# Kernel tuning notes

Measured on AMD Instinct MI355X. Metric: run time of the kernel, lower is better.

## Reference

```python
import jax, jax.numpy as jnp
import numpy as np

EPS = 1e-5  # BatchNorm2d eps
NEG_SLOPE = 0.01  # LeakyReLU default


def _cconv_bn_act(x, W, b, g, beta):
    # Complex 1x1 conv + per-part BatchNorm (batch stats) + LeakyReLU.
    # x: [B,2,C,F,T]; W: [2,C,C] (real, imag); b, g, beta: [2,C]
    xr, xi = x[:, 0], x[:, 1]
    yr = (jnp.einsum('oc,bcft->boft', W[0], xr)
          - jnp.einsum('oc,bcft->boft', W[1], xi) + b[0][None, :, None, None])
    yi = (jnp.einsum('oc,bcft->boft', W[0], xi)
          + jnp.einsum('oc,bcft->boft', W[1], xr) + b[1][None, :, None, None])

    def bn(y, gg, bb):
        mu = y.mean(axis=(0, 2, 3), keepdims=True)
        var = y.var(axis=(0, 2, 3), keepdims=True)  # biased, as torch BN normalization
        return (y - mu) / jnp.sqrt(var + EPS) * gg[None, :, None, None] + bb[None, :, None, None]

    yr = jax.nn.leaky_relu(bn(yr, g[0], beta[0]), NEG_SLOPE)
    yi = jax.nn.leaky_relu(bn(yi, g[1], beta[1]), NEG_SLOPE)
    return jnp.stack((yr, yi), axis=1)


def _complex_attn(q, k, v):
    # q,k,v: [B,2,N,D]; magnitude-based scores, softmax over dim=1 of [B,N,N]
    # (faithful to nn.Softmax(dim=1) applied to a 3-D score tensor).
    qr, qi = q[:, 0], q[:, 1]
    kr, ki = k[:, 0], k[:, 1]
    sr = jnp.einsum('bnd,bmd->bnm', qr, kr) + jnp.einsum('bnd,bmd->bnm', qi, ki)
    si = jnp.einsum('bnd,bmd->bnm', qi, kr) - jnp.einsum('bnd,bmd->bnm', qr, ki)
    a = jax.nn.softmax(jnp.sqrt(sr * sr + si * si), axis=1)
    outr = jnp.einsum('bnm,bmd->bnd', a, v[:, 0])
    outi = jnp.einsum('bnm,bmd->bnd', a, v[:, 1])
    return jnp.stack((outr, outi), axis=1)


def _forward(P, Q, W, b, g, beta):
    B, _, C, F, T = P.shape
    # --- Time-axis attention: tokens = T frames, feature dim = C*F ---
    qt = _cconv_bn_act(Q, W[0], b[0], g[0], beta[0])
    kt = _cconv_bn_act(P, W[1], b[1], g[1], beta[1])
    vt = _cconv_bn_act(P, W[2], b[2], g[2], beta[2])

    def to_time(x):  # [B,2,C,F,T] -> [B,2,T,C*F]
        return x.reshape(B, 2, C * F, T).transpose(0, 1, 3, 2)

    ot = _complex_attn(to_time(qt), to_time(kt), to_time(vt))
    ot = ot.transpose(0, 1, 3, 2).reshape(B, 2, C, F, T)

    # --- Freq-axis attention: tokens = F bins, feature dim = C*T ---
    qf = _cconv_bn_act(Q, W[3], b[3], g[3], beta[3])
    kf = _cconv_bn_act(P, W[4], b[4], g[4], beta[4])
    vf = _cconv_bn_act(P, W[5], b[5], g[5], beta[5])

    def to_freq(x):  # [B,2,C,F,T] -> [B,2,F,C*T]
        return x.transpose(0, 1, 3, 2, 4).reshape(B, 2, F, C * T)

    of = _complex_attn(to_freq(qf), to_freq(kf), to_freq(vf))
    of = of.reshape(B, 2, F, C, T).transpose(0, 1, 3, 2, 4)

    # Combine the two attention axes (truncated top-level module; see notes).
    return ot + of


def setup_inputs():
    key = jax.random.key(0)
    ks = jax.random.split(key, 4)
    B, C, F, T = 2, 64, 256, 256
    P = jax.random.normal(ks[0], (B, 2, C, F, T), dtype=jnp.float32)
    Q = jax.random.normal(ks[1], (B, 2, C, F, T), dtype=jnp.float32)
    # 6 branches: [time-q, time-k, time-v, freq-q, freq-k, freq-v]
    W = jax.random.normal(ks[2], (6, 2, C, C), dtype=jnp.float32) / np.sqrt(C).astype(np.float32)
    b = jax.random.normal(ks[3], (6, 2, C), dtype=jnp.float32) * 0.01
    g = jnp.ones((6, 2, C), dtype=jnp.float32)
    beta = jnp.zeros((6, 2, C), dtype=jnp.float32)
    return {"P": P, "Q": Q, "W": W, "b": b, "g": g, "beta": beta}


def reference(P, Q, W, b, g, beta):
    return _forward(P, Q, W, b, g, beta)
```

## Files before the change

kernel.cpp:

```cpp
#include <hip/hip_runtime.h>
#include <math.h>

#define SS 65536
#define PLANE 4194304
#define TEN_ELEMS 16777216
#define NBUCKET 64

typedef __bf16 bf16x8 __attribute__((ext_vector_type(8)));
typedef __bf16 bf16x4v __attribute__((ext_vector_type(4)));
typedef float  f32x4  __attribute__((ext_vector_type(4)));

__device__ inline f32x4 mfma16(bf16x8 a, bf16x8 b, f32x4 c) {
  return __builtin_amdgcn_mfma_f32_16x16x32_bf16(a, b, c, 0, 0, 0);
}
__device__ inline bf16x8 neg8(bf16x8 v) {
  union { bf16x8 b; unsigned u[4]; } t; t.b = v;
#pragma unroll
  for (int i = 0; i < 4; ++i) t.u[i] ^= 0x80008000u;
  return t.b;
}
__device__ inline float bnlrelu(float v, float sc, float sh) {
  float t = fmaf(v, sc, sh);
  return t > 0.f ? t : 0.01f * t;
}

__device__ inline int swz(int r, int g) {
  return r * 40 + (((g ^ (r >> 2) ^ (r >> 4)) & 3) << 3);
}

__global__ __launch_bounds__(256) void cconv_mfma(
    const float* __restrict__ x, const float* __restrict__ Wj,
    const float* __restrict__ bias, float* __restrict__ y,
    float* __restrict__ part)
{
  __shared__ __align__(16) __bf16 sBh[64 * 136];
  __shared__ __align__(16) __bf16 sBl[64 * 136];
  const int tid = threadIdx.x;
  const int b = blockIdx.y;
  const int s0 = blockIdx.x << 6;
  const int bkt = (blockIdx.x & (NBUCKET - 1)) * 768;
  const int w = tid >> 6, q = (tid >> 4) & 3, ln = tid & 15;

  bf16x8 ah[2][4], al[2][4];
#pragma unroll
  for (int mt = 0; mt < 2; ++mt) {
    int row = w * 32 + mt * 16 + ln;
    int po = row >> 6, co = row & 63;
#pragma unroll
    for (int ks = 0; ks < 4; ++ks) {
      bf16x8 vh, vl;
#pragma unroll
      for (int j = 0; j < 8; ++j) {
        int k = ks * 32 + q * 8 + j;
        int pi = k >> 6, c = k & 63;
        float v = Wj[((po ^ pi) << 12) + co * 64 + c];
        if (po == 0 && pi == 1) v = -v;
        __bf16 h = (__bf16)v;
        vh[j] = h;
        vl[j] = (__bf16)(v - (float)h);
      }
      ah[mt][ks] = vh; al[mt][ks] = vl;
    }
  }

#pragma unroll
  for (int ph = 0; ph < 2; ++ph) {
    int pc = ph * 64 + (tid & 63);
    const float* rowp = x + (size_t)(b * 128 + pc) * SS + s0;
#pragma unroll
    for (int sh2 = 0; sh2 < 2; ++sh2)
#pragma unroll
      for (int sc2 = 0; sc2 < 2; ++sc2) {
        int sl = ((tid >> 6) << 3) + sh2 * 32 + sc2 * 4;
        float4 rd = *(const float4*)&rowp[sl];
        float vv[4] = {rd.x, rd.y, rd.z, rd.w};
#pragma unroll
        for (int e = 0; e < 4; ++e) {
          __bf16 h = (__bf16)vv[e];
          sBh[(sl + e) * 136 + pc] = h;
          sBl[(sl + e) * 136 + pc] = (__bf16)(vv[e] - (float)h);
        }
      }
  }
  __syncthreads();

  f32x4 zero = {0.f, 0.f, 0.f, 0.f};
  f32x4 acc[2][4];
#pragma unroll
  for (int mt = 0; mt < 2; ++mt)
#pragma unroll
    for (int nt = 0; nt < 4; ++nt) acc[mt][nt] = zero;

#pragma unroll
  for (int ks = 0; ks < 4; ++ks) {
    bf16x8 bh[4], bl[4];
#pragma unroll
    for (int nt = 0; nt < 4; ++nt) {
      int off = (nt * 16 + ln) * 136 + ks * 32 + q * 8;
      bh[nt] = *(const bf16x8*)&sBh[off];
      bl[nt] = *(const bf16x8*)&sBl[off];
    }
#pragma unroll
    for (int mt = 0; mt < 2; ++mt)
#pragma unroll
      for (int nt = 0; nt < 4; ++nt) {
        acc[mt][nt] = mfma16(ah[mt][ks], bh[nt], acc[mt][nt]);
        acc[mt][nt] = mfma16(ah[mt][ks], bl[nt], acc[mt][nt]);
        acc[mt][nt] = mfma16(al[mt][ks], bh[nt], acc[mt][nt]);
      }
  }

#pragma unroll
  for (int mt = 0; mt < 2; ++mt) {
    int rowb = w * 32 + mt * 16 + q * 4;
#pragma unroll
    for (int r = 0; r < 4; ++r) {
      float bv = bias[rowb + r];
      float vs[4];
      float sm = 0.f, sq = 0.f;
#pragma unroll
      for (int nt = 0; nt < 4; ++nt) {
        float v = acc[mt][nt][r] + bv;
        vs[nt] = v; sm += v; sq += v * v;
      }
#pragma unroll
      for (int off = 1; off < 16; off <<= 1) {
        sm += __shfl_xor(sm, off, 64);
        sq += __shfl_xor(sq, off, 64);
      }
      if (ln == 0) {
        atomicAdd(&part[bkt + (rowb + r) * 2 + 0], sm);
        atomicAdd(&part[bkt + (rowb + r) * 2 + 1], sq);
      }
#pragma unroll
      for (int nt = 0; nt < 4; ++nt)
        y[(size_t)((b << 7) + rowb + r) * SS + s0 + nt * 16 + ln] = vs[nt];
    }
  }
}

__global__ void bn_finalize(const float* __restrict__ buckets,
                            const float* __restrict__ g,
                            const float* __restrict__ beta, int goff,
                            float* __restrict__ scale, float* __restrict__ shift)
{
  int i = blockIdx.x * 256 + threadIdx.x;
  if (i >= 384) return;
  int role = i >> 7, pc = i & 127;
  float sm = 0.f, sq = 0.f;
  const float* bp = buckets + role * 256 + pc * 2;
#pragma unroll 4
  for (int k = 0; k < NBUCKET; ++k) {
    sm += bp[k * 768 + 0];
    sq += bp[k * 768 + 1];
  }
  const float inv = 1.f / 131072.f;
  float mu = sm * inv;
  float var = sq * inv - mu * mu;
  float istd = rsqrtf(var + 1e-5f);
  float gg = g[goff + role * 128 + pc];
  float bb = beta[goff + role * 128 + pc];
  float sc = gg * istd;
  scale[i] = sc;
  shift[i] = bb - mu * sc;
}

__global__ __launch_bounds__(256) void qk_prep(
    float* __restrict__ y0, float* __restrict__ y1,
    const float* __restrict__ scale, const float* __restrict__ shift, int freq)
{
  const int g = blockIdx.x;
  const int b2p = blockIdx.y;
  const int role = blockIdx.z;
  float* y = role ? y1 : y0;
  const int p = b2p & 1;
  const int c = g >> 3;
  const float sc = scale[role * 128 + p * 64 + c];
  const float sh = shift[role * 128 + p * 64 + c];
  const int tid = threadIdx.x;
  const size_t base = (size_t)b2p * PLANE + (size_t)g * 8192;
  __bf16* yo = (__bf16*)y;

  float v[32];
  if (freq) {
    size_t off = base + (size_t)tid * 32;
#pragma unroll
    for (int r = 0; r < 8; ++r) {
      float4 t4 = *(const float4*)&y[off + r * 4];
      v[r * 4 + 0] = t4.x; v[r * 4 + 1] = t4.y;
      v[r * 4 + 2] = t4.z; v[r * 4 + 3] = t4.w;
    }
    size_t ob = off * 2;
#pragma unroll
    for (int r = 0; r < 4; ++r) {
      bf16x8 hv, lv;
#pragma unroll
      for (int e = 0; e < 8; ++e) {
        float t = bnlrelu(v[r * 8 + e], sc, sh);
        __bf16 hh = (__bf16)t;
        hv[e] = hh; lv[e] = (__bf16)(t - (float)hh);
      }
      *(bf16x8*)&yo[ob + r * 8]      = hv;
      *(bf16x8*)&yo[ob + 32 + r * 8] = lv;
    }
  } else {
    __shared__ __align__(16) float sT[32 * 256];
#pragma unroll
    for (int r = 0; r < 8; ++r) {
      int u = tid + (r << 8);
      int tok4 = u & 63, j = u >> 6;
      float4 t4 = *(const float4*)&y[base + j * 256 + tok4 * 4];
      *(float4*)&sT[j * 256 + ((tok4 ^ j) << 2)] = t4;
    }
    __syncthreads();
    const int tok = tid;
#pragma unroll
    for (int j = 0; j < 32; ++j)
      v[j] = sT[j * 256 + (((tok >> 2) ^ j) << 2) + (tok & 3)];
    size_t ob = (base + (size_t)tok * 32) * 2;
#pragma unroll
    for (int r = 0; r < 4; ++r) {
      bf16x8 hv, lv;
#pragma unroll
      for (int e = 0; e < 8; ++e) {
        float t = bnlrelu(v[r * 8 + e], sc, sh);
        __bf16 hh = (__bf16)t;
        hv[e] = hh; lv[e] = (__bf16)(t - (float)hh);
      }
      *(bf16x8*)&yo[ob + r * 8]      = hv;
      *(bf16x8*)&yo[ob + 32 + r * 8] = lv;
    }
  }
}

__global__ __launch_bounds__(256) void score_mfma(
    const __bf16* __restrict__ qt, const __bf16* __restrict__ kt,
    float* __restrict__ SR, float* __restrict__ SI, int freq)
{
  __shared__ __align__(16) __bf16 sQh[2 * 128 * 40], sQl[2 * 128 * 40];
  __shared__ __align__(16) __bf16 sKh[2 * 64 * 40],  sKl[2 * 64 * 40];
  const int tid = threadIdx.x;
  const int sid = blockIdx.x + (blockIdx.y << 3) + (blockIdx.z << 8);
  const int kk = sid & 7, tt = sid >> 3;
  const int n0 = (kk & 1) << 7;
  const int b  = (kk >> 1) & 1;
  const int m0 = (tt & 3) << 6;
  const int d0 = (((kk >> 2) << 4) + (tt >> 2)) << 9;
  const int g0 = d0 >> 5;
  const int w = tid >> 6, q4 = (tid >> 4) & 3, ln = tid & 15;
  const size_t pb = (size_t)(b * 2) * (2 * PLANE);

  f32x4 zero = {0.f, 0.f, 0.f, 0.f};
  f32x4 accr[2][4], acci[2][4];
#pragma unroll
  for (int st = 0; st < 2; ++st)
#pragma unroll
    for (int mt = 0; mt < 4; ++mt) { accr[st][mt] = zero; acci[st][mt] = zero; }

  for (int ch = 0; ch < 16; ++ch) {
    const int g = g0 + ch;
    int Gq, Gk, Gstep;
    if (freq) {
      int cc = g >> 3, gg = g & 7;
      Gq = cc * 2048 + n0 * 8 + gg;
      Gk = cc * 2048 + m0 * 8 + gg;
      Gstep = 8;
    } else {
      Gq = g * 256 + n0;
      Gk = g * 256 + m0;
      Gstep = 1;
    }
#pragma unroll
    for (int r = 0; r < 4; ++r) {
      int u = tid + (r << 8);
      int g_ = u & 3, tok = (u >> 2) & 127, p = u >> 9;
      size_t a = pb + (size_t)p * (2 * PLANE) +
                 (size_t)(Gq + tok * Gstep) * 64 + (g_ << 3);
      int dst = swz(p * 128 + tok, g_);
      *(bf16x8*)&sQh[dst] = *(const bf16x8*)&qt[a];
      *(bf16x8*)&sQl[dst] = *(const bf16x8*)&qt[a + 32];
    }
#pragma unroll
    for (int r = 0; r < 2; ++r) {
      int u = tid + (r << 8);
      int g_ = u & 3, tok = (u >> 2) & 63, p = u >> 8;
      size_t a = pb + (size_t)p * (2 * PLANE) +
                 (size_t)(Gk + tok * Gstep) * 64 + (g_ << 3);
      int dst = swz(p * 64 + tok, g_);
      *(bf16x8*)&sKh[dst] = *(const bf16x8*)&kt[a];
      *(bf16x8*)&sKl[dst] = *(const bf16x8*)&kt[a + 32];
    }
    __syncthreads();

    bf16x8 qh[2][2], ql2[2][2], nqh[2], nql[2];
#pragma unroll
    for (int st = 0; st < 2; ++st) {
      int tokn = w * 32 + st * 16 + ln;
#pragma unroll
      for (int p = 0; p < 2; ++p) {
        int off = swz(p * 128 + tokn, q4);
        qh[st][p]  = *(const bf16x8*)&sQh[off];
        ql2[st][p] = *(const bf16x8*)&sQl[off];
      }
      nqh[st] = neg8(qh[st][0]);
      nql[st] = neg8(ql2[st][0]);
    }
#pragma unroll
    for (int mt = 0; mt < 4; ++mt) {
      int tk = mt * 16 + ln;
      int offr = swz(tk, q4), offi = swz(64 + tk, q4);
      bf16x8 krh = *(const bf16x8*)&sKh[offr];
      bf16x8 krl = *(const bf16x8*)&sKl[offr];
      bf16x8 kih = *(const bf16x8*)&sKh[offi];
      bf16x8 kil = *(const bf16x8*)&sKl[offi];
#pragma unroll
      for (int st = 0; st < 2; ++st) {
        f32x4 ar = accr[st][mt], ai = acci[st][mt];
        ar = mfma16(qh[st][0], krh, ar);
        ar = mfma16(qh[st][0], krl, ar);
        ar = mfma16(ql2[st][0], krh, ar);
        ar = mfma16(qh[st][1], kih, ar);
        ar = mfma16(qh[st][1], kil, ar);
        ar = mfma16(ql2[st][1], kih, ar);
        ai = mfma16(qh[st][1], krh, ai);
        ai = mfma16(qh[st][1], krl, ai);
        ai = mfma16(ql2[st][1], krh, ai);
        ai = mfma16(nqh[st], kih, ai);
        ai = mfma16(nqh[st], kil, ai);
        ai = mfma16(nql[st], kih, ai);
        accr[st][mt] = ar; acci[st][mt] = ai;
      }
    }
    __syncthreads();
  }

#pragma unroll
  for (int st = 0; st < 2; ++st)
#pragma unroll
    for (int mt = 0; mt < 4; ++mt)
#pragma unroll
      for (int r = 0; r < 4; ++r) {
        int n = n0 + w * 32 + st * 16 + q4 * 4 + r;
        int m = m0 + mt * 16 + ln;
        int idx = (b << 16) + (n << 8) + m;
        atomicAdd(&SR[idx], accr[st][mt][r]);
        atomicAdd(&SI[idx], acci[st][mt][r]);
      }
}

__global__ __launch_bounds__(256) void softmax_kernel(
    const float* __restrict__ sr, const float* __restrict__ si,
    float* __restrict__ am)
{
  const int m = blockIdx.x & 255;
  const int b = blockIdx.x >> 8;
  const int n = threadIdx.x;
  const int idx = (b << 16) + (n << 8) + m;
  float vr = sr[idx], vi = si[idx];
  float mag = sqrtf(vr * vr + vi * vi);
  __shared__ float wmax[4];
  __shared__ float wsum[4];
  float mx = mag;
  #pragma unroll
  for (int off = 1; off < 64; off <<= 1)
    mx = fmaxf(mx, __shfl_xor(mx, off, 64));
  if ((threadIdx.x & 63) == 0) wmax[threadIdx.x >> 6] = mx;
  __syncthreads();
  mx = fmaxf(fmaxf(wmax[0], wmax[1]), fmaxf(wmax[2], wmax[3]));
  float e = expf(mag - mx);
  float sm = e;
  #pragma unroll
  for (int off = 1; off < 64; off <<= 1)
    sm += __shfl_xor(sm, off, 64);
  if ((threadIdx.x & 63) == 0) wsum[threadIdx.x >> 6] = sm;
  __syncthreads();
  float tot = wsum[0] + wsum[1] + wsum[2] + wsum[3];
  am[idx] = e / tot;
}

__global__ __launch_bounds__(256) void vt_convert(
    const float* __restrict__ y2, const float* __restrict__ scale,
    const float* __restrict__ shift, __bf16* __restrict__ vh,
    __bf16* __restrict__ vl)
{
  size_t i = ((size_t)blockIdx.x * 256 + threadIdx.x) << 2;
  int idx = 256 + (int)((i >> 16) & 127);
  float sc = scale[idx], sh = shift[idx];
  float4 v = *(const float4*)&y2[i];
  float vv[4] = {v.x, v.y, v.z, v.w};
  bf16x4v h, l;
#pragma unroll
  for (int e = 0; e < 4; ++e) {
    float t = bnlrelu(vv[e], sc, sh);
    __bf16 hh = (__bf16)t;
    h[e] = hh; l[e] = (__bf16)(t - (float)hh);
  }
  *(bf16x4v*)&vh[i] = h;
  *(bf16x4v*)&vl[i] = l;
}

__global__ __launch_bounds__(256) void vt_transpose(
    const float* __restrict__ y2, const float* __restrict__ scale,
    const float* __restrict__ shift, __bf16* __restrict__ vh,
    __bf16* __restrict__ vl)
{
  __shared__ float sT[64 * 65];
  const int tid = threadIdx.x;
  const int bpc = blockIdx.y;
  const int bp = bpc >> 6, c = bpc & 63;
  const int f0 = (blockIdx.x >> 2) << 6, t0 = (blockIdx.x & 3) << 6;
  const float sc = scale[256 + (bp & 1) * 64 + c];
  const float sh = shift[256 + (bp & 1) * 64 + c];
  const float* src = y2 + (size_t)bp * PLANE + (size_t)c * SS;
#pragma unroll
  for (int r = 0; r < 4; ++r) {
    int fl = (tid >> 4) + (r << 4);
    int tl = (tid & 15) << 2;
    float4 v = *(const float4*)&src[(f0 + fl) * 256 + t0 + tl];
    sT[fl * 65 + tl + 0] = bnlrelu(v.x, sc, sh);
    sT[fl * 65 + tl + 1] = bnlrelu(v.y, sc, sh);
    sT[fl * 65 + tl + 2] = bnlrelu(v.z, sc, sh);
    sT[fl * 65 + tl + 3] = bnlrelu(v.w, sc, sh);
  }
  __syncthreads();
  __bf16* dsth = vh + (((size_t)bp * 16384 + c * 256) << 8);
  __bf16* dstl = vl + (((size_t)bp * 16384 + c * 256) << 8);
#pragma unroll
  for (int r = 0; r < 4; ++r) {
    int tl = (tid >> 4) + (r << 4);
    int fl = (tid & 15) << 2;
    bf16x4v h, l;
#pragma unroll
    for (int e = 0; e < 4; ++e) {
      float vv = sT[(fl + e) * 65 + tl];
      __bf16 hh = (__bf16)vv;
      h[e] = hh; l[e] = (__bf16)(vv - (float)hh);
    }
    *(bf16x4v*)&dsth[(size_t)(t0 + tl) * 256 + f0 + fl] = h;
    *(bf16x4v*)&dstl[(size_t)(t0 + tl) * 256 + f0 + fl] = l;
  }
}

__global__ __launch_bounds__(256) void av_mfma(
    const float* __restrict__ am, const __bf16* __restrict__ vth,
    const __bf16* __restrict__ vtl, float* __restrict__ out, int freq)
{
  __shared__ __align__(16) char smem[55296];
  __bf16* sVh = (__bf16*)smem;
  __bf16* sVl = (__bf16*)(smem + 18432);
  __bf16* sAh = (__bf16*)(smem + 36864);
  __bf16* sAl = (__bf16*)(smem + 46080);
  const int tid = threadIdx.x;
  const int d0 = blockIdx.x << 7;
  const int n0 = blockIdx.y << 6;
  const int bp = blockIdx.z, b = bp >> 1;
  const int w = tid >> 6, q = (tid >> 4) & 3, ln = tid & 15;
  const __bf16* vhp = vth + (((size_t)bp * 16384 + d0) << 8);
  const __bf16* vlp = vtl + (((size_t)bp * 16384 + d0) << 8);
  float* op = out + (size_t)bp * PLANE;

  f32x4 zero = {0.f, 0.f, 0.f, 0.f};
  f32x4 acc[2][4];
#pragma unroll
  for (int mt = 0; mt < 2; ++mt)
#pragma unroll
    for (int nt = 0; nt < 4; ++nt) acc[mt][nt] = zero;

  for (int m0 = 0; m0 < 256; m0 += 64) {
#pragma unroll
    for (int r = 0; r < 4; ++r) {
      int u = tid + (r << 8);
      int dl = u >> 3, g = (u & 7) << 3;
      *(bf16x8*)&sVh[dl * 72 + g] = *(const bf16x8*)&vhp[dl * 256 + m0 + g];
      *(bf16x8*)&sVl[dl * 72 + g] = *(const bf16x8*)&vlp[dl * 256 + m0 + g];
    }
#pragma unroll
    for (int r = 0; r < 4; ++r) {
      int u = tid + (r << 8);
      int mj = (u & 15) << 2, nl = u >> 4;
      float4 v4 = *(const float4*)&am[(b << 16) + ((n0 + nl) << 8) + m0 + mj];
      float vv[4] = {v4.x, v4.y, v4.z, v4.w};
      bf16x4v h, l;
#pragma unroll
      for (int e = 0; e < 4; ++e) {
        __bf16 hh = (__bf16)vv[e];
        h[e] = hh; l[e] = (__bf16)(vv[e] - (float)hh);
      }
      *(bf16x4v*)&sAh[nl * 72 + mj] = h;
      *(bf16x4v*)&sAl[nl * 72 + mj] = l;
    }
    __syncthreads();

#pragma unroll
    for (int ks = 0; ks < 2; ++ks) {
      bf16x8 vhf[2], vlf[2], ahf[4], alf[4];
#pragma unroll
      for (int mt = 0; mt < 2; ++mt) {
        int off = (w * 32 + mt * 16 + ln) * 72 + ks * 32 + q * 8;
        vhf[mt] = *(const bf16x8*)&sVh[off];
        vlf[mt] = *(const bf16x8*)&sVl[off];
      }
#pragma unroll
      for (int nt = 0; nt < 4; ++nt) {
        int off = (nt * 16 + ln) * 72 + ks * 32 + q * 8;
        ahf[nt] = *(const bf16x8*)&sAh[off];
        alf[nt] = *(const bf16x8*)&sAl[off];
      }
#pragma unroll
      for (int mt = 0; mt < 2; ++mt)
#pragma unroll
        for (int nt = 0; nt < 4; ++nt) {
          f32x4 a = acc[mt][nt];
          a = mfma16(vhf[mt], ahf[nt], a);
          a = mfma16(vhf[mt], alf[nt], a);
          a = mfma16(vlf[mt], ahf[nt], a);
          acc[mt][nt] = a;
        }
    }
    __syncthreads();
  }

  if (!freq) {
#pragma unroll
    for (int mt = 0; mt < 2; ++mt)
#pragma unroll
      for (int nt = 0; nt < 4; ++nt)
#pragma unroll
        for (int r = 0; r < 4; ++r) {
          int row = d0 + w * 32 + mt * 16 + q * 4 + r;
          op[(size_t)row * 256 + n0 + nt * 16 + ln] = acc[mt][nt][r];
        }
  } else {
    float* sO = (float*)smem;
#pragma unroll
    for (int mt = 0; mt < 2; ++mt)
#pragma unroll
      for (int nt = 0; nt < 4; ++nt)
#pragma unroll
        for (int r = 0; r < 4; ++r)
          sO[(w * 32 + mt * 16 + q * 4 + r) * 65 + nt * 16 + ln] = acc[mt][nt][r];
    __syncthreads();
    const int c = d0 >> 8, t0 = d0 & 255;
    const int dl = (tid & 31) << 2, nb = tid >> 5;
#pragma unroll
    for (int r = 0; r < 8; ++r) {
      int n = nb + (r << 3);
      float4 wv = make_float4(sO[(dl + 0) * 65 + n], sO[(dl + 1) * 65 + n],
                              sO[(dl + 2) * 65 + n], sO[(dl + 3) * 65 + n]);
      size_t addr = (size_t)c * SS + (size_t)(n0 + n) * 256 + t0 + dl;
      float4 o = *(float4*)&op[addr];
      wv.x += o.x; wv.y += o.y; wv.z += o.z; wv.w += o.w;
      *(float4*)&op[addr] = wv;
    }
  }
}

extern "C" void kernel_launch(void* const* d_in, const int* in_sizes, int n_in,
                              void* d_out, int out_size, void* d_ws, size_t ws_size,
                              hipStream_t stream) {
  const float* P    = (const float*)d_in[0];
  const float* Q    = (const float*)d_in[1];
  const float* W    = (const float*)d_in[2];
  const float* bias = (const float*)d_in[3];
  const float* g    = (const float*)d_in[4];
  const float* beta = (const float*)d_in[5];
  float* out = (float*)d_out;
  float* ws  = (float*)d_ws;

  float* Y0    = ws;
  float* Y1    = Y0 + TEN_ELEMS;
  float* Y2    = Y1 + TEN_ELEMS;
  float* SR    = Y2 + TEN_ELEMS;
  float* SI    = SR + 131072;
  float* AM    = SI + 131072;
  float* BUCK  = AM + 131072;
  float* SCALE = BUCK + NBUCKET * 768;
  float* SHIFT = SCALE + 384;

  __bf16* VTh = (__bf16*)Y0;
  __bf16* VTl = VTh + TEN_ELEMS;

  for (int phase = 0; phase < 2; ++phase) {
    int j0 = phase * 3;
    int freq = phase;
    hipMemsetAsync(BUCK, 0, NBUCKET * 768 * sizeof(float), stream);
    cconv_mfma<<<dim3(1024, 2), 256, 0, stream>>>(
        Q, W + (size_t)j0 * 8192, bias + j0 * 128, Y0, BUCK);
    cconv_mfma<<<dim3(1024, 2), 256, 0, stream>>>(
        P, W + (size_t)(j0 + 1) * 8192, bias + (j0 + 1) * 128, Y1, BUCK + 256);
    cconv_mfma<<<dim3(1024, 2), 256, 0, stream>>>(
        P, W + (size_t)(j0 + 2) * 8192, bias + (j0 + 2) * 128, Y2, BUCK + 512);
    bn_finalize<<<2, 256, 0, stream>>>(BUCK, g, beta, j0 * 128, SCALE, SHIFT);
    qk_prep<<<dim3(512, 4, 2), 256, 0, stream>>>(Y0, Y1, SCALE, SHIFT, freq);
    hipMemsetAsync(SR, 0, 2 * 131072 * sizeof(float), stream);
    score_mfma<<<dim3(8, 32, 2), 256, 0, stream>>>(
        (const __bf16*)Y0, (const __bf16*)Y1, SR, SI, freq);
    softmax_kernel<<<512, 256, 0, stream>>>(SR, SI, AM);
    if (!freq)
      vt_convert<<<16384, 256, 0, stream>>>(Y2, SCALE, SHIFT, VTh, VTl);
    else
      vt_transpose<<<dim3(16, 256), 256, 0, stream>>>(Y2, SCALE, SHIFT, VTh, VTl);
    av_mfma<<<dim3(128, 4, 4), 256, 0, stream>>>(AM, VTh, VTl, out, freq);
  }
}
```

Measured before the change: 836.6 us.

## Compute BN stats analytically from input covariance and fuse BN+act into conv epilogue

BatchNorm statistics for each 1x1 complex conv are now derived from a per-input channel covariance matrix and mean (W·C·Wᵀ), computed once for P and Q by a new MFMA kernel, so the conv kernels no longer need atomics or a second pass. The conv epilogue applies BN scale/shift plus LeakyReLU directly and writes bf16 hi/lo split tensors in the layout the score and AV kernels expect. This removes the qk_prep and vt_convert passes and their fp32 round trips. The bias is dropped because it cancels under batch normalization. Variance via E[y²]-mu² from a bf16-split covariance may lose some precision.

New measurement: 1.417 ms. 1.69x slower.

```diff
diff --git a/kernel.cpp b/kernel.cpp
--- a/kernel.cpp
+++ b/kernel.cpp
@@ -4,7 +4,7 @@
 #define SS 65536
 #define PLANE 4194304
 #define TEN_ELEMS 16777216
-#define NBUCKET 64
+#define NSAMP 131072.0f
 
 typedef __bf16 bf16x8 __attribute__((ext_vector_type(8)));
 typedef __bf16 bf16x4v __attribute__((ext_vector_type(4)));
@@ -28,17 +28,144 @@
   return r * 40 + (((g ^ (r >> 2) ^ (r >> 4)) & 3) << 3);
 }
 
+__global__ __launch_bounds__(256) void stats_cov(
+    const float* __restrict__ xQ, const float* __restrict__ xP,
+    float* __restrict__ Cq, float* __restrict__ Cp,
+    float* __restrict__ mq, float* __restrict__ mp)
+{
+  __shared__ __align__(16) __bf16 sXh[128 * 72];
+  __shared__ __align__(16) __bf16 sXl[128 * 72];
+  const int tid = threadIdx.x;
+  const int swin = blockIdx.x;
+  const int b = blockIdx.y;
+  const float* x = blockIdx.z ? xP : xQ;
+  float* C = blockIdx.z ? Cp : Cq;
+  float* m = blockIdx.z ? mp : mq;
+  const int w = tid >> 6, q = (tid >> 4) & 3, ln = tid & 15;
+  const int pcb = tid >> 4;
+  const int s4 = (tid & 15) * 4;
+
+  f32x4 zero = {0.f, 0.f, 0.f, 0.f};
+  f32x4 acc[2][8];
+#pragma unroll
+  for (int mt = 0; mt < 2; ++mt)
+#pragma unroll
+    for (int nt = 0; nt < 8; ++nt) acc[mt][nt] = zero;
+  float msum[8] = {0.f, 0.f, 0.f, 0.f, 0.f, 0.f, 0.f, 0.f};
+
+  for (int it = 0; it < 16; ++it) {
+    const int sbase = swin * 1024 + it * 64;
+#pragma unroll
+    for (int r = 0; r < 8; ++r) {
+      int pc = pcb + r * 16;
+      float4 v4 = *(const float4*)&x[(size_t)(b * 128 + pc) * SS + sbase + s4];
+      msum[r] += v4.x + v4.y + v4.z + v4.w;
+      float vv[4] = {v4.x, v4.y, v4.z, v4.w};
+      bf16x4v hv, lv;
+#pragma unroll
+      for (int e = 0; e < 4; ++e) {
+        __bf16 h = (__bf16)vv[e];
+        hv[e] = h; lv[e] = (__bf16)(vv[e] - (float)h);
+      }
+      *(bf16x4v*)&sXh[pc * 72 + s4] = hv;
+      *(bf16x4v*)&sXl[pc * 72 + s4] = lv;
+    }
+    __syncthreads();
+#pragma unroll
+    for (int ks = 0; ks < 2; ++ks) {
+      bf16x8 ah[2], al[2];
+#pragma unroll
+      for (int mt = 0; mt < 2; ++mt) {
+        int ra = w * 32 + mt * 16 + ln;
+        ah[mt] = *(const bf16x8*)&sXh[ra * 72 + ks * 32 + q * 8];
+        al[mt] = *(const bf16x8*)&sXl[ra * 72 + ks * 32 + q * 8];
+      }
+#pragma unroll
+      for (int nt = 0; nt < 8; ++nt) {
+        int rb = nt * 16 + ln;
+        bf16x8 bh = *(const bf16x8*)&sXh[rb * 72 + ks * 32 + q * 8];
+        bf16x8 bl = *(const bf16x8*)&sXl[rb * 72 + ks * 32 + q * 8];
+#pragma unroll
+        for (int mt = 0; mt < 2; ++mt) {
+          f32x4 a = acc[mt][nt];
+          a = mfma16(ah[mt], bh, a);
+          a = mfma16(ah[mt], bl, a);
+          a = mfma16(al[mt], bh, a);
+          acc[mt][nt] = a;
+        }
+      }
+    }
+    __syncthreads();
+  }
+#pragma unroll
+  for (int r = 0; r < 8; ++r) atomicAdd(&m[pcb + r * 16], msum[r]);
+#pragma unroll
+  for (int mt = 0; mt < 2; ++mt)
+#pragma unroll
+    for (int nt = 0; nt < 8; ++nt)
+#pragma unroll
+      for (int r = 0; r < 4; ++r) {
+        int row = w * 32 + mt * 16 + q * 4 + r;
+        int col = nt * 16 + ln;
+        atomicAdd(&C[row * 128 + col], acc[mt][nt][r]);
+      }
+}
+
+__global__ void bn_precompute(
+    const float* __restrict__ Cq, const float* __restrict__ Cp,
+    const float* __restrict__ mq, const float* __restrict__ mp,
+    const float* __restrict__ W, const float* __restrict__ g,
+    const float* __restrict__ beta,
+    float* __restrict__ scale6, float* __restrict__ shift6)
+{
+  const int rr = blockIdx.x >> 7;
+  const int o  = blockIdx.x & 127;
+  const int i  = threadIdx.x;
+  const float* C = (rr % 3 == 0) ? Cq : Cp;
+  const float* m = (rr % 3 == 0) ? mq : mp;
+  const int po = o >> 6, co = o & 63;
+  const int pi = i >> 6, ci = i & 63;
+  float wv = W[rr * 8192 + ((po ^ pi) << 12) + co * 64 + ci];
+  if (po == 0 && pi == 1) wv = -wv;
+  __shared__ float sW[128];
+  sW[i] = wv;
+  __syncthreads();
+  float t = 0.f;
+  const float* crow = C + i * 128;
+#pragma unroll 8
+  for (int j = 0; j < 128; ++j) t += crow[j] * sW[j];
+  float pv = wv * t;
+  float pm = wv * m[i];
+#pragma unroll
+  for (int off = 1; off < 64; off <<= 1) {
+    pv += __shfl_xor(pv, off, 64);
+    pm += __shfl_xor(pm, off, 64);
+  }
+  __shared__ float red[4];
+  if ((i & 63) == 0) { red[(i >> 6) * 2] = pv; red[(i >> 6) * 2 + 1] = pm; }
+  __syncthreads();
+  if (i == 0) {
+    float v = red[0] + red[2];
+    float wm = red[1] + red[3];
+    float muT = wm / NSAMP;
+    float var = v / NSAMP - muT * muT;
+    float sc = g[rr * 128 + o] * rsqrtf(var + 1e-5f);
+    scale6[rr * 128 + o] = sc;
+    shift6[rr * 128 + o] = beta[rr * 128 + o] - muT * sc;
+  }
+}
+
 __global__ __launch_bounds__(256) void cconv_mfma(
     const float* __restrict__ x, const float* __restrict__ Wj,
-    const float* __restrict__ bias, float* __restrict__ y,
-    float* __restrict__ part)
+    const float* __restrict__ scale, const float* __restrict__ shiftp,
+    void* __restrict__ outA, void* __restrict__ outB, int mode, int freq)
 {
-  __shared__ __align__(16) __bf16 sBh[64 * 136];
-  __shared__ __align__(16) __bf16 sBl[64 * 136];
+  __shared__ __align__(16) char smemBlk[34816];
+  __bf16* sBh = (__bf16*)smemBlk;
+  __bf16* sBl = (__bf16*)(smemBlk + 17408);
   const int tid = threadIdx.x;
   const int b = blockIdx.y;
   const int s0 = blockIdx.x << 6;
-  const int bkt = (blockIdx.x & (NBUCKET - 1)) * 768;
   const int w = tid >> 6, q = (tid >> 4) & 3, ln = tid & 15;
 
   bf16x8 ah[2][4], al[2][4];
@@ -110,132 +237,113 @@
       }
   }
 
-#pragma unroll
-  for (int mt = 0; mt < 2; ++mt) {
-    int rowb = w * 32 + mt * 16 + q * 4;
+  float scv[2][4], shv[2][4];
+#pragma unroll
+  for (int mt = 0; mt < 2; ++mt)
 #pragma unroll
     for (int r = 0; r < 4; ++r) {
-      float bv = bias[rowb + r];
-      float vs[4];
-      float sm = 0.f, sq = 0.f;
-#pragma unroll
-      for (int nt = 0; nt < 4; ++nt) {
-        float v = acc[mt][nt][r] + bv;
-        vs[nt] = v; sm += v; sq += v * v;
-      }
-#pragma unroll
-      for (int off = 1; off < 16; off <<= 1) {
-        sm += __shfl_xor(sm, off, 64);
-        sq += __shfl_xor(sq, off, 64);
-      }
-      if (ln == 0) {
-        atomicAdd(&part[bkt + (rowb + r) * 2 + 0], sm);
-        atomicAdd(&part[bkt + (rowb + r) * 2 + 1], sq);
-      }
+      int row = w * 32 + mt * 16 + q * 4 + r;
+      scv[mt][r] = scale[row];
+      shv[mt][r] = shiftp[row];
+    }
+
+  if (mode == 2) {
+    float* y = (float*)outA;
+#pragma unroll
+    for (int mt = 0; mt < 2; ++mt)
+#pragma unroll
+      for (int r = 0; r < 4; ++r) {
+        int row = w * 32 + mt * 16 + q * 4 + r;
+#pragma unroll
+        for (int nt = 0; nt < 4; ++nt)
+          y[(size_t)(b * 128 + row) * SS + s0 + nt * 16 + ln] =
+              bnlrelu(acc[mt][nt][r], scv[mt][r], shv[mt][r]);
+      }
+  } else if (mode == 1) {
+    __bf16* vh = (__bf16*)outA;
+    __bf16* vl = (__bf16*)outB;
+    const int f = s0 >> 8, t0 = s0 & 255;
+#pragma unroll
+    for (int mt = 0; mt < 2; ++mt)
+#pragma unroll
+      for (int r = 0; r < 4; ++r) {
+        int row = w * 32 + mt * 16 + q * 4 + r;
+        int p = row >> 6, c = row & 63;
+        size_t rbase = ((size_t)((b * 2 + p) * 16384 + c * 256 + f)) * 256 + t0;
+#pragma unroll
+        for (int nt = 0; nt < 4; ++nt) {
+          float v = bnlrelu(acc[mt][nt][r], scv[mt][r], shv[mt][r]);
+          __bf16 h = (__bf16)v;
+          vh[rbase + nt * 16 + ln] = h;
+          vl[rbase + nt * 16 + ln] = (__bf16)(v - (float)h);
+        }
+      }
+  } else {
+    __syncthreads();
+    float* sT = (float*)smemBlk;
+#pragma unroll
+    for (int mt = 0; mt < 2; ++mt)
 #pragma unroll
       for (int nt = 0; nt < 4; ++nt)
-        y[(size_t)((b << 7) + rowb + r) * SS + s0 + nt * 16 + ln] = vs[nt];
-    }
-  }
-}
-
-__global__ void bn_finalize(const float* __restrict__ buckets,
-                            const float* __restrict__ g,
-                            const float* __restrict__ beta, int goff,
-                            float* __restrict__ scale, float* __restrict__ shift)
-{
-  int i = blockIdx.x * 256 + threadIdx.x;
-  if (i >= 384) return;
-  int role = i >> 7, pc = i & 127;
-  float sm = 0.f, sq = 0.f;
-  const float* bp = buckets + role * 256 + pc * 2;
-#pragma unroll 4
-  for (int k = 0; k < NBUCKET; ++k) {
-    sm += bp[k * 768 + 0];
-    sq += bp[k * 768 + 1];
-  }
-  const float inv = 1.f / 131072.f;
-  float mu = sm * inv;
-  float var = sq * inv - mu * mu;
-  float istd = rsqrtf(var + 1e-5f);
-  float gg = g[goff + role * 128 + pc];
-  float bb = beta[goff + role * 128 + pc];
-  float sc = gg * istd;
-  scale[i] = sc;
-  shift[i] = bb - mu * sc;
-}
-
-__global__ __launch_bounds__(256) void qk_prep(
-    float* __restrict__ y0, float* __restrict__ y1,
-    const float* __restrict__ scale, const float* __restrict__ shift, int freq)
-{
-  const int g = blockIdx.x;
-  const int b2p = blockIdx.y;
-  const int role = blockIdx.z;
-  float* y = role ? y1 : y0;
-  const int p = b2p & 1;
-  const int c = g >> 3;
-  const float sc = scale[role * 128 + p * 64 + c];
-  const float sh = shift[role * 128 + p * 64 + c];
-  const int tid = threadIdx.x;
-  const size_t base = (size_t)b2p * PLANE + (size_t)g * 8192;
-  __bf16* yo = (__bf16*)y;
-
-  float v[32];
-  if (freq) {
-    size_t off = base + (size_t)tid * 32;
-#pragma unroll
-    for (int r = 0; r < 8; ++r) {
-      float4 t4 = *(const float4*)&y[off + r * 4];
-      v[r * 4 + 0] = t4.x; v[r * 4 + 1] = t4.y;
-      v[r * 4 + 2] = t4.z; v[r * 4 + 3] = t4.w;
-    }
-    size_t ob = off * 2;
-#pragma unroll
-    for (int r = 0; r < 4; ++r) {
-      bf16x8 hv, lv;
+#pragma unroll
+        for (int r = 0; r < 4; ++r)
+          sT[(nt * 16 + ln) * 133 + (w * 32 + mt * 16 + q * 4 + r)] =
+              bnlrelu(acc[mt][nt][r], scv[mt][r], shv[mt][r]);
+    __syncthreads();
+    const int pch = tid >> 6, tl = tid & 63;
+    float vv[32];
+#pragma unroll
+    for (int j2 = 0; j2 < 8; ++j2)
+      *(f32x4*)&vv[j2 * 4] = *(const f32x4*)&sT[tl * 133 + pch * 32 + j2 * 4];
+    bf16x8 hh[4], ll[4];
+#pragma unroll
+    for (int j2 = 0; j2 < 4; ++j2)
 #pragma unroll
       for (int e = 0; e < 8; ++e) {
-        float t = bnlrelu(v[r * 8 + e], sc, sh);
-        __bf16 hh = (__bf16)t;
-        hv[e] = hh; lv[e] = (__bf16)(t - (float)hh);
-      }
-      *(bf16x8*)&yo[ob + r * 8]      = hv;
-      *(bf16x8*)&yo[ob + 32 + r * 8] = lv;
-    }
-  } else {
-    __shared__ __align__(16) float sT[32 * 256];
-#pragma unroll
-    for (int r = 0; r < 8; ++r) {
-      int u = tid + (r << 8);
-      int tok4 = u & 63, j = u >> 6;
-      float4 t4 = *(const float4*)&y[base + j * 256 + tok4 * 4];
-      *(float4*)&sT[j * 256 + ((tok4 ^ j) << 2)] = t4;
-    }
-    __syncthreads();
-    const int tok = tid;
-#pragma unroll
-    for (int j = 0; j < 32; ++j)
-      v[j] = sT[j * 256 + (((tok >> 2) ^ j) << 2) + (tok & 3)];
-    size_t ob = (base + (size_t)tok * 32) * 2;
-#pragma unroll
-    for (int r = 0; r < 4; ++r) {
-      bf16x8 hv, lv;
-#pragma unroll
-      for (int e = 0; e < 8; ++e) {
-        float t = bnlrelu(v[r * 8 + e], sc, sh);
-        __bf16 hh = (__bf16)t;
-        hv[e] = hh; lv[e] = (__bf16)(t - (float)hh);
-      }
-      *(bf16x8*)&yo[ob + r * 8]      = hv;
-      *(bf16x8*)&yo[ob + 32 + r * 8] = lv;
+        float v = vv[j2 * 8 + e];
+        __bf16 h = (__bf16)v;
+        hh[j2][e] = h; ll[j2][e] = (__bf16)(v - (float)h);
+      }
+    __bf16* out = (__bf16*)outA;
+    if (!freq) {
+      const int p = pch >> 1, ch2 = pch & 1;
+      int chunk = (s0 >> 8) * 2 + ch2;
+      int tok = (s0 & 255) + tl;
+      size_t a = (size_t)(b * 2 + p) * (2 * (size_t)PLANE) +
+                 ((size_t)chunk * 256 + tok) * 64;
+#pragma unroll
+      for (int j2 = 0; j2 < 4; ++j2) {
+        *(bf16x8*)&out[a + j2 * 8]      = hh[j2];
+        *(bf16x8*)&out[a + 32 + j2 * 8] = ll[j2];
+      }
+    } else {
+      __syncthreads();
+      __bf16* sP = (__bf16*)smemBlk;
+      __bf16* me = sP + tid * 64;
+#pragma unroll
+      for (int j2 = 0; j2 < 4; ++j2) {
+        *(bf16x8*)&me[j2 * 8]      = hh[j2];
+        *(bf16x8*)&me[32 + j2 * 8] = ll[j2];
+      }
+      __syncthreads();
+#pragma unroll
+      for (int r2 = 0; r2 < 8; ++r2) {
+        int u = tid + (r2 << 8);
+        int g2 = u >> 3, piece = u & 7;
+        int pch2 = g2 >> 6, t2 = g2 & 63;
+        int chunk = ((s0 & 255) + t2) * 2 + (pch2 & 1);
+        int tok = s0 >> 8;
+        size_t a = (size_t)(b * 2 + (pch2 >> 1)) * (2 * (size_t)PLANE) +
+                   ((size_t)chunk * 256 + tok) * 64 + piece * 8;
+        *(bf16x8*)&out[a] = *(const bf16x8*)&sP[(size_t)u * 8];
+      }
     }
   }
 }
 
 __global__ __launch_bounds__(256) void score_mfma(
     const __bf16* __restrict__ qt, const __bf16* __restrict__ kt,
-    float* __restrict__ SR, float* __restrict__ SI, int freq)
+    float* __restrict__ SR, float* __restrict__ SI)
 {
   __shared__ __align__(16) __bf16 sQh[2 * 128 * 40], sQl[2 * 128 * 40];
   __shared__ __align__(16) __bf16 sKh[2 * 64 * 40],  sKl[2 * 64 * 40];
@@ -245,10 +353,9 @@
   const int n0 = (kk & 1) << 7;
   const int b  = (kk >> 1) & 1;
   const int m0 = (tt & 3) << 6;
-  const int d0 = (((kk >> 2) << 4) + (tt >> 2)) << 9;
-  const int g0 = d0 >> 5;
+  const int g0 = (((kk >> 2) << 4) + (tt >> 2)) << 4;
   const int w = tid >> 6, q4 = (tid >> 4) & 3, ln = tid & 15;
-  const size_t pb = (size_t)(b * 2) * (2 * PLANE);
+  const size_t pb = (size_t)(b * 2) * (2 * (size_t)PLANE);
 
   f32x4 zero = {0.f, 0.f, 0.f, 0.f};
   f32x4 accr[2][4], acci[2][4];
@@ -259,23 +366,14 @@
 
   for (int ch = 0; ch < 16; ++ch) {
     const int g = g0 + ch;
-    int Gq, Gk, Gstep;
-    if (freq) {
-      int cc = g >> 3, gg = g & 7;
-      Gq = cc * 2048 + n0 * 8 + gg;
-      Gk = cc * 2048 + m0 * 8 + gg;
-      Gstep = 8;
-    } else {
-      Gq = g * 256 + n0;
-      Gk = g * 256 + m0;
-      Gstep = 1;
-    }
+    const int Gq = g * 256 + n0;
+    const int Gk = g * 256 + m0;
 #pragma unroll
     for (int r = 0; r < 4; ++r) {
       int u = tid + (r << 8);
       int g_ = u & 3, tok = (u >> 2) & 127, p = u >> 9;
-      size_t a = pb + (size_t)p * (2 * PLANE) +
-                 (size_t)(Gq + tok * Gstep) * 64 + (g_ << 3);
+      size_t a = pb + (size_t)p * (2 * (size_t)PLANE) +
+                 (size_t)(Gq + tok) * 64 + (g_ << 3);
       int dst = swz(p * 128 + tok, g_);
       *(bf16x8*)&sQh[dst] = *(const bf16x8*)&qt[a];
       *(bf16x8*)&sQl[dst] = *(const bf16x8*)&qt[a + 32];
@@ -284,8 +382,8 @@
     for (int r = 0; r < 2; ++r) {
       int u = tid + (r << 8);
       int g_ = u & 3, tok = (u >> 2) & 63, p = u >> 8;
-      size_t a = pb + (size_t)p * (2 * PLANE) +
-                 (size_t)(Gk + tok * Gstep) * 64 + (g_ << 3);
+      size_t a = pb + (size_t)p * (2 * (size_t)PLANE) +
+                 (size_t)(Gk + tok) * 64 + (g_ << 3);
       int dst = swz(p * 64 + tok, g_);
       *(bf16x8*)&sKh[dst] = *(const bf16x8*)&kt[a];
       *(bf16x8*)&sKl[dst] = *(const bf16x8*)&kt[a + 32];
@@ -378,30 +476,8 @@
   am[idx] = e / tot;
 }
 
-__global__ __launch_bounds__(256) void vt_convert(
-    const float* __restrict__ y2, const float* __restrict__ scale,
-    const float* __restrict__ shift, __bf16* __restrict__ vh,
-    __bf16* __restrict__ vl)
-{
-  size_t i = ((size_t)blockIdx.x * 256 + threadIdx.x) << 2;
-  int idx = 256 + (int)((i >> 16) & 127);
-  float sc = scale[idx], sh = shift[idx];
-  float4 v = *(const float4*)&y2[i];
-  float vv[4] = {v.x, v.y, v.z, v.w};
-  bf16x4v h, l;
-#pragma unroll
-  for (int e = 0; e < 4; ++e) {
-    float t = bnlrelu(vv[e], sc, sh);
-    __bf16 hh = (__bf16)t;
-    h[e] = hh; l[e] = (__bf16)(t - (float)hh);
-  }
-  *(bf16x4v*)&vh[i] = h;
-  *(bf16x4v*)&vl[i] = l;
-}
-
 __global__ __launch_bounds__(256) void vt_transpose(
-    const float* __restrict__ y2, const float* __restrict__ scale,
-    const float* __restrict__ shift, __bf16* __restrict__ vh,
+    const float* __restrict__ y2, __bf16* __restrict__ vh,
     __bf16* __restrict__ vl)
 {
   __shared__ float sT[64 * 65];
@@ -409,18 +485,16 @@
   const int bpc = blockIdx.y;
   const int bp = bpc >> 6, c = bpc & 63;
   const int f0 = (blockIdx.x >> 2) << 6, t0 = (blockIdx.x & 3) << 6;
-  const float sc = scale[256 + (bp & 1) * 64 + c];
-  const float sh = shift[256 + (bp & 1) * 64 + c];
   const float* src = y2 + (size_t)bp * PLANE + (size_t)c * SS;
 #pragma unroll
   for (int r = 0; r < 4; ++r) {
     int fl = (tid >> 4) + (r << 4);
     int tl = (tid & 15) << 2;
     float4 v = *(const float4*)&src[(f0 + fl) * 256 + t0 + tl];
-    sT[fl * 65 + tl + 0] = bnlrelu(v.x, sc, sh);
-    sT[fl * 65 + tl + 1] = bnlrelu(v.y, sc, sh);
-    sT[fl * 65 + tl + 2] = bnlrelu(v.z, sc, sh);
-    sT[fl * 65 + tl + 3] = bnlrelu(v.w, sc, sh);
+    sT[fl * 65 + tl + 0] = v.x;
+    sT[fl * 65 + tl + 1] = v.y;
+    sT[fl * 65 + tl + 2] = v.z;
+    sT[fl * 65 + tl + 3] = v.w;
   }
   __syncthreads();
   __bf16* dsth = vh + (((size_t)bp * 16384 + c * 256) << 8);
@@ -561,7 +635,6 @@
   const float* P    = (const float*)d_in[0];
   const float* Q    = (const float*)d_in[1];
   const float* W    = (const float*)d_in[2];
-  const float* bias = (const float*)d_in[3];
   const float* g    = (const float*)d_in[4];
   const float* beta = (const float*)d_in[5];
   float* out = (float*)d_out;
@@ -573,33 +646,52 @@
   float* SR    = Y2 + TEN_ELEMS;
   float* SI    = SR + 131072;
   float* AM    = SI + 131072;
-  float* BUCK  = AM + 131072;
-  float* SCALE = BUCK + NBUCKET * 768;
-  float* SHIFT = SCALE + 384;
-
-  __bf16* VTh = (__bf16*)Y0;
-  __bf16* VTl = VTh + TEN_ELEMS;
+  float* CQ    = AM + 131072;
+  float* CP    = CQ + 16384;
+  float* MQ    = CP + 16384;
+  float* MP    = MQ + 128;
+  float* SCALE6 = MP + 128;
+  float* SHIFT6 = SCALE6 + 768;
+
+  hipMemsetAsync(CQ, 0, (2 * 16384 + 2 * 128) * sizeof(float), stream);
+  stats_cov<<<dim3(64, 2, 2), 256, 0, stream>>>(Q, P, CQ, CP, MQ, MP);
+  bn_precompute<<<768, 128, 0, stream>>>(CQ, CP, MQ, MP, W, g, beta,
+                                         SCALE6, SHIFT6);
 
   for (int phase = 0; phase < 2; ++phase) {
     int j0 = phase * 3;
     int freq = phase;
-    hipMemsetAsync(BUCK, 0, NBUCKET * 768 * sizeof(float), stream);
     cconv_mfma<<<dim3(1024, 2), 256, 0, stream>>>(
-        Q, W + (size_t)j0 * 8192, bias + j0 * 128, Y0, BUCK);
+        Q, W + (size_t)j0 * 8192, SCALE6 + j0 * 128, SHIFT6 + j0 * 128,
+        Y0, nullptr, 0, freq);
     cconv_mfma<<<dim3(1024, 2), 256, 0, stream>>>(
-        P, W + (size_t)(j0 + 1) * 8192, bias + (j0 + 1) * 128, Y1, BUCK + 256);
-    cconv_mfma<<<dim3(1024, 2), 256, 0, stream>>>(
-        P, W + (size_t)(j0 + 2) * 8192, bias + (j0 + 2) * 128, Y2, BUCK + 512);
-    bn_finalize<<<2, 256, 0, stream>>>(BUCK, g, beta, j0 * 128, SCALE, SHIFT);
-    qk_prep<<<dim3(512, 4, 2), 256, 0, stream>>>(Y0, Y1, SCALE, SHIFT, freq);
+        P, W + (size_t)(j0 + 1) * 8192, SCALE6 + (j0 + 1) * 128,
+        SHIFT6 + (j0 + 1) * 128, Y1, nullptr, 0, freq);
+    if (!freq)
+      cconv_mfma<<<dim3(1024, 2), 256, 0, stream>>>(
+          P, W + (size_t)(j0 + 2) * 8192, SCALE6 + (j0 + 2) * 128,
+          SHIFT6 + (j0 + 2) * 128, Y2, (char*)Y2 + (size_t)TEN_ELEMS * 2, 1, 0);
+    else
+      cconv_mfma<<<dim3(1024, 2), 256, 0, stream>>>(
+          P, W + (size_t)(j0 + 2) * 8192, SCALE6 + (j0 + 2) * 128,
+          SHIFT6 + (j0 + 2) * 128, Y2, nullptr, 2, 1);
+
     hipMemsetAsync(SR, 0, 2 * 131072 * sizeof(float), stream);
     score_mfma<<<dim3(8, 32, 2), 256, 0, stream>>>(
-        (const __bf16*)Y0, (const __bf16*)Y1, SR, SI, freq);
+        (const __bf16*)Y0, (const __bf16*)Y1, SR, SI);
     softmax_kernel<<<512, 256, 0, stream>>>(SR, SI, AM);
-    if (!freq)
-      vt_convert<<<16384, 256, 0, stream>>>(Y2, SCALE, SHIFT, VTh, VTl);
-    else
-      vt_transpose<<<dim3(16, 256), 256, 0, stream>>>(Y2, SCALE, SHIFT, VTh, VTl);
+
+    const __bf16* VTh;
+    const __bf16* VTl;
+    if (!freq) {
+      VTh = (const __bf16*)Y2;
+      VTl = (const __bf16*)((char*)Y2 + (size_t)TEN_ELEMS * 2);
+    } else {
+      vt_transpose<<<dim3(16, 256), 256, 0, stream>>>(
+          Y2, (__bf16*)Y0, (__bf16*)((char*)Y0 + (size_t)TEN_ELEMS * 2));
+      VTh = (const __bf16*)Y0;
+      VTl = (const __bf16*)((char*)Y0 + (size_t)TEN_ELEMS * 2);
+    }
     av_mfma<<<dim3(128, 4, 4), 256, 0, stream>>>(AM, VTh, VTl, out, freq);
   }
 }
```
